# Optimization experiments

Measured on AMD Instinct MI355X. Metric: run time of the kernel, lower is better.

## Reference

```python
import jax, jax.numpy as jnp
import numpy as np

B, S, H, I, SI, E, TOPK = 2, 1024, 1024, 512, 2048, 8, 2


def setup_inputs() -> dict:
    key = jax.random.key(0)
    ks = jax.random.split(key, 8)
    w = 0.02
    return {
        "hidden_states": jax.random.normal(ks[0], (B, S, H), jnp.float32),
        "router_weight": jax.random.normal(ks[1], (E, H), jnp.float32) * w,
        "gate_up_proj": jax.random.normal(ks[2], (E, 2 * I, H), jnp.float32) * w,
        "down_proj": jax.random.normal(ks[3], (E, H, I), jnp.float32) * w,
        "shared_gate_w": jax.random.normal(ks[4], (SI, H), jnp.float32) * w,
        "shared_up_w": jax.random.normal(ks[5], (SI, H), jnp.float32) * w,
        "shared_down_w": jax.random.normal(ks[6], (H, SI), jnp.float32) * w,
        "shared_expert_gate_w": jax.random.normal(ks[7], (1, H), jnp.float32) * w,
    }


def reference(hidden_states, router_weight, gate_up_proj, down_proj,
              shared_gate_w, shared_up_w, shared_down_w, shared_expert_gate_w):
    b, s, h = hidden_states.shape
    x = hidden_states.reshape(-1, h)  # [T, H]

    # shared expert (SwiGLU)
    shared = (jax.nn.silu(x @ shared_gate_w.T) * (x @ shared_up_w.T)) @ shared_down_w.T  # [T, H]

    # top-k softmax router (softmax in fp32, renormalized top-k weights)
    logits = x @ router_weight.T  # [T, E]
    probs = jax.nn.softmax(logits.astype(jnp.float32), axis=-1)
    top_v, top_i = jax.lax.top_k(probs, TOPK)
    top_v = (top_v / jnp.sum(top_v, axis=-1, keepdims=True)).astype(logits.dtype)  # [T, K]

    # combine weights per (token, expert): sum over k of routing weight * one_hot
    cw = jnp.sum(jax.nn.one_hot(top_i, E, dtype=top_v.dtype) * top_v[..., None], axis=1)  # [T, E]

    # grouped-expert SwiGLU (dense compute, masked combine == gather/scatter math)
    gu = jnp.einsum('th,eih->eti', x, gate_up_proj)  # [E, T, 2I]
    gate, up = jnp.split(gu, 2, axis=-1)
    act = jax.nn.silu(gate) * up  # [E, T, I]
    per_expert = jnp.einsum('eti,ehi->eth', act, down_proj)  # [E, T, H]
    expert_out = jnp.einsum('eth,te->th', per_expert, cw)  # [T, H]

    out = expert_out + jax.nn.sigmoid(x @ shared_expert_gate_w.T) * shared
    return out.reshape(b, s, h)
```

## Files before the change

kernel.cpp:

```cpp
#include <hip/hip_runtime.h>

#define T_TOK 2048
#define H_DIM 1024
#define I_DIM 512
#define SI_DIM 2048
#define E_NUM 8
#define NSLOT 4096

typedef __attribute__((ext_vector_type(8))) short short8;
typedef __attribute__((ext_vector_type(4))) float floatx4;

__device__ inline unsigned short f2bf(float f) {
  unsigned u = __builtin_bit_cast(unsigned, f);
  u = (u + 0x7FFFu + ((u >> 16) & 1u)) >> 16;
  return (unsigned short)u;
}
__device__ inline float bf2f(unsigned short u) {
  return __builtin_bit_cast(float, (unsigned)u << 16);
}

__device__ inline void gl_lds16(const void* g, void* l) {
  __builtin_amdgcn_global_load_lds(
      (const __attribute__((address_space(1))) unsigned int*)g,
      (__attribute__((address_space(3))) unsigned int*)l, 16, 0, 0);
}

__global__ __launch_bounds__(256) void cast_router(
    const float* __restrict__ x, const float* __restrict__ rw,
    const float* __restrict__ segw,
    const float* __restrict__ s1, const float* __restrict__ s2,
    const float* __restrict__ s3, const float* __restrict__ s4,
    const float* __restrict__ s5,
    unsigned short* __restrict__ d0, unsigned short* __restrict__ d1,
    unsigned short* __restrict__ d2, unsigned short* __restrict__ d3,
    unsigned short* __restrict__ d4, unsigned short* __restrict__ d5,
    int* __restrict__ top2, float2* __restrict__ w01, float* __restrict__ sg) {
  const int bid = blockIdx.x;
  if (bid < 512) {
    int t = bid * 4 + (threadIdx.x >> 6);
    int lane = threadIdx.x & 63;
    const float* xt = x + (long)t * H_DIM;
    float xv[16];
#pragma unroll
    for (int j = 0; j < 16; ++j) xv[j] = xt[j * 64 + lane];
    float dots[9];
#pragma unroll
    for (int e = 0; e < 8; ++e) {
      const float* w = rw + e * H_DIM;
      float s = 0.f;
#pragma unroll
      for (int j = 0; j < 16; ++j) s += xv[j] * w[j * 64 + lane];
      dots[e] = s;
    }
    {
      float s = 0.f;
#pragma unroll
      for (int j = 0; j < 16; ++j) s += xv[j] * segw[j * 64 + lane];
      dots[8] = s;
    }
#pragma unroll
    for (int off = 32; off > 0; off >>= 1) {
#pragma unroll
      for (int e = 0; e < 9; ++e) dots[e] += __shfl_xor(dots[e], off, 64);
    }
    if (lane == 0) {
      int e0 = 0;
      for (int e = 1; e < 8; ++e)
        if (dots[e] > dots[e0]) e0 = e;
      int e1 = (e0 == 0) ? 1 : 0;
      for (int e = 0; e < 8; ++e)
        if (e != e0 && dots[e] > dots[e1]) e1 = e;
      float p1 = expf(dots[e1] - dots[e0]);
      top2[t] = e0 | (e1 << 8);
      w01[t] = make_float2(1.f / (1.f + p1), p1 / (1.f + p1));
      sg[t] = 1.f / (1.f + expf(-dots[8]));
    }
  } else {
    long g = (long)(bid - 512) * 256 + threadIdx.x;
    const float* s;
    unsigned short* d;
    long off;
    if (g < 524288L)       { s = x;  d = d0; off = g; }
    else if (g < 2621440L) { s = s1; d = d1; off = g - 524288L; }
    else if (g < 3670016L) { s = s2; d = d2; off = g - 2621440L; }
    else if (g < 4194304L) { s = s3; d = d3; off = g - 3670016L; }
    else if (g < 4718592L) { s = s4; d = d4; off = g - 4194304L; }
    else                   { s = s5; d = d5; off = g - 4718592L; }
    float4 v = ((const float4*)s)[off];
    ushort4 o;
    o.x = f2bf(v.x); o.y = f2bf(v.y); o.z = f2bf(v.z); o.w = f2bf(v.w);
    ((ushort4*)d)[off] = o;
  }
}

__global__ __launch_bounds__(256) void build_lists(
    const int* __restrict__ top2, int* __restrict__ cnt, int* __restrict__ ebase,
    int* __restrict__ slot_token, int* __restrict__ tok_slot) {
  const int e = blockIdx.x;
  const int tid = threadIdx.x;
  const int lane = tid & 63, wid = tid >> 6;
  __shared__ int wsum[4], wbelow[4];
  const int base_t = tid * 8;
  int mk[8], kk[8];
  int c = 0, below = 0;
#pragma unroll
  for (int j = 0; j < 8; ++j) {
    int p = top2[base_t + j];
    int e0 = p & 0xFF, e1 = (p >> 8) & 0xFF;
    below += (e0 < e) + (e1 < e);
    int m = 0, k = 0;
    if (e0 == e) { m = 1; k = 0; }
    else if (e1 == e) { m = 1; k = 1; }
    mk[j] = m; kk[j] = k;
    c += m;
  }
  int inc = c;
#pragma unroll
  for (int off = 1; off < 64; off <<= 1) {
    int n = __shfl_up(inc, off, 64);
    if (lane >= off) inc += n;
  }
  int bsum = below;
#pragma unroll
  for (int off = 32; off > 0; off >>= 1) bsum += __shfl_xor(bsum, off, 64);
  if (lane == 63) wsum[wid] = inc;
  if (lane == 0) wbelow[wid] = bsum;
  __syncthreads();
  int woff = 0;
#pragma unroll
  for (int i = 0; i < 4; ++i)
    if (i < wid) woff += wsum[i];
  int baseE = wbelow[0] + wbelow[1] + wbelow[2] + wbelow[3];
  int pos = baseE + woff + inc - c;
#pragma unroll
  for (int j = 0; j < 8; ++j) {
    if (mk[j]) {
      slot_token[pos] = base_t + j;
      tok_slot[2 * (base_t + j) + kk[j]] = pos;
      pos++;
    }
  }
  if (tid == 255) cnt[e] = woff + inc;
  if (tid == 0) ebase[e] = baseE;
}

template <bool GATHER, int BN>
__device__ __forceinline__ void swiglu_body(
    char* smem, int bx, int by, int e,
    const unsigned short* __restrict__ A, const unsigned short* __restrict__ Bg,
    const unsigned short* __restrict__ Bu, unsigned short* __restrict__ Out,
    const int* __restrict__ slot_token, const int* __restrict__ cnt,
    const int* __restrict__ ebase, int N, int K, long estrideB) {
  constexpr int BM = 128, BK = 32;
  constexpr int NT = BN / 32;
  constexpr int BCH = BN / 64;
  constexpr int ATILE = BM * BK;
  constexpr int BTILE = BN * BK;
  const int tid = threadIdx.x;
  const int lane = tid & 63;
  const int wid = tid >> 6;
  const int wm = wid & 1;
  const int wn = wid >> 1;
  const int m0 = by * BM;
  const int n0 = bx * BN;
  int Meff = 0, baseE = 0;
  if (GATHER) {
    Meff = cnt[e];
    if (m0 >= Meff) return;
    baseE = ebase[e];
  }
  const unsigned short* BgE = Bg + (long)e * estrideB;
  const unsigned short* BuE = Bu + (long)e * estrideB;

  unsigned short* As = (unsigned short*)smem;
  unsigned short* Bgs = As + 2 * ATILE;
  unsigned short* Bus = Bgs + 2 * BTILE;

  const int lrow = lane >> 2;
  const int lcol = (((lane & 3) ^ ((lrow >> 1) & 3)) << 4);

  const char* aP[2];
#pragma unroll
  for (int i = 0; i < 2; ++i) {
    int m = m0 + wid * 32 + i * 16 + lrow;
    long row;
    if (GATHER) {
      int mm = (m < Meff - 1) ? m : (Meff - 1);
      row = slot_token[baseE + mm];
    } else {
      row = m;
    }
    aP[i] = (const char*)A + row * (long)(K * 2) + lcol;
  }
  const char* bgP[BCH];
  const char* buP[BCH];
#pragma unroll
  for (int i = 0; i < BCH; ++i) {
    int n = n0 + wid * (16 * BCH) + i * 16 + lrow;
    bgP[i] = (const char*)BgE + (long)n * (K * 2) + lcol;
    buP[i] = (const char*)BuE + (long)n * (K * 2) + lcol;
  }

  floatx4 accG[4][NT], accU[4][NT];
  floatx4 zero = {0.f, 0.f, 0.f, 0.f};
#pragma unroll
  for (int i = 0; i < 4; ++i)
#pragma unroll
    for (int j = 0; j < NT; ++j) { accG[i][j] = zero; accU[i][j] = zero; }

  const int ar = lane & 15;
  const int aksw = (((lane >> 4) ^ ((ar >> 1) & 3)) << 3);

  auto stage = [&](int p, int k0) {
#pragma unroll
    for (int i = 0; i < 2; ++i)
      gl_lds16(aP[i] + (long)k0 * 2, &As[p * ATILE + (wid * 32 + i * 16) * BK]);
#pragma unroll
    for (int i = 0; i < BCH; ++i) {
      gl_lds16(bgP[i] + (long)k0 * 2,
               &Bgs[p * BTILE + (wid * 16 * BCH + i * 16) * BK]);
      gl_lds16(buP[i] + (long)k0 * 2,
               &Bus[p * BTILE + (wid * 16 * BCH + i * 16) * BK]);
    }
  };

  stage(0, 0);
  const int NI = K / BK;
  for (int i = 0; i < NI; ++i) {
    __syncthreads();
    if (i + 1 < NI) stage((i + 1) & 1, (i + 1) * BK);
    const unsigned short* Ab = &As[(i & 1) * ATILE];
    const unsigned short* Gb = &Bgs[(i & 1) * BTILE];
    const unsigned short* Ub = &Bus[(i & 1) * BTILE];
    short8 af[4], bgf[NT], buf2[NT];
#pragma unroll
    for (int tm = 0; tm < 4; ++tm)
      af[tm] = *(const short8*)&Ab[(wm * 64 + tm * 16 + ar) * BK + aksw];
#pragma unroll
    for (int tn = 0; tn < NT; ++tn) {
      bgf[tn] = *(const short8*)&Gb[(wn * (BN / 2) + tn * 16 + ar) * BK + aksw];
      buf2[tn] = *(const short8*)&Ub[(wn * (BN / 2) + tn * 16 + ar) * BK + aksw];
    }
#pragma unroll
    for (int tm = 0; tm < 4; ++tm)
#pragma unroll
      for (int tn = 0; tn < NT; ++tn) {
        accG[tm][tn] = __builtin_amdgcn_mfma_f32_16x16x32_bf16(af[tm], bgf[tn], accG[tm][tn], 0, 0, 0);
        accU[tm][tn] = __builtin_amdgcn_mfma_f32_16x16x32_bf16(af[tm], buf2[tn], accU[tm][tn], 0, 0, 0);
      }
  }

#pragma unroll
  for (int tm = 0; tm < 4; ++tm)
#pragma unroll
    for (int tn = 0; tn < NT; ++tn)
#pragma unroll
      for (int r = 0; r < 4; ++r) {
        int row = m0 + wm * 64 + tm * 16 + (lane >> 4) * 4 + r;
        int col = n0 + wn * (BN / 2) + tn * 16 + (lane & 15);
        if (!GATHER || row < Meff) {
          float g = accG[tm][tn][r];
          float u = accU[tm][tn][r];
          float act = g / (1.f + expf(-g)) * u;
          Out[(long)(baseE + row) * N + col] = f2bf(act);
        }
      }
}

__global__ __launch_bounds__(256, 2) void swiglu_fused(
    const unsigned short* __restrict__ xb, const unsigned short* __restrict__ sgate,
    const unsigned short* __restrict__ sup, unsigned short* __restrict__ act_s,
    const unsigned short* __restrict__ gup, unsigned short* __restrict__ act_e,
    const int* __restrict__ slot_token, const int* __restrict__ cnt,
    const int* __restrict__ ebase) {
  __shared__ __align__(16) char smem[49152];
  int bid = blockIdx.x;
  if (bid < 256) {
    swiglu_body<false, 128>(smem, bid & 15, bid >> 4, 0, xb, sgate, sup, act_s,
                            nullptr, nullptr, nullptr, SI_DIM, H_DIM, 0);
  } else {
    int b2 = bid - 256;
    int e = b2 >> 7;
    int rem = b2 & 127;
    swiglu_body<true, 64>(smem, rem & 7, rem >> 3, e, xb, gup,
                          gup + (long)I_DIM * H_DIM, act_e, slot_token, cnt,
                          ebase, I_DIM, H_DIM, (long)2 * I_DIM * H_DIM);
  }
}

template <int MODE>
__device__ __forceinline__ void down_body(
    char* smem, int bx, int by, int e,
    const unsigned short* __restrict__ A, const unsigned short* __restrict__ B,
    float* __restrict__ OutF, unsigned short* __restrict__ OutB,
    const int* __restrict__ ebase, const int* __restrict__ cnt,
    int N, int Kstride, int kbeg, int kcnt, long estrideB) {
  constexpr int BM = 128, BN = 128, BK = 32;
  constexpr int ATILE = BM * BK;
  constexpr int BTILE = BN * BK;
  const int tid = threadIdx.x;
  const int lane = tid & 63;
  const int wid = tid >> 6;
  const int wm = wid & 1;
  const int wn = wid >> 1;
  const int m0 = by * BM;
  const int n0 = bx * BN;
  int Meff = 0, baseE = 0;
  if (MODE == 1) {
    Meff = cnt[e];
    if (m0 >= Meff) return;
    baseE = ebase[e];
  }
  const unsigned short* BE = B + (long)e * estrideB;

  unsigned short* As = (unsigned short*)smem;
  unsigned short* Bs = As + 2 * ATILE;

  const int lrow = lane >> 2;
  const int lcol = (((lane & 3) ^ ((lrow >> 1) & 3)) << 4);

  const char* aP[2];
  const char* bP[2];
#pragma unroll
  for (int i = 0; i < 2; ++i) {
    int m = m0 + wid * 32 + i * 16 + lrow;
    long arow;
    if (MODE == 1) {
      int mm = (m < Meff - 1) ? m : (Meff - 1);
      arow = baseE + mm;
    } else {
      arow = m;
    }
    aP[i] = (const char*)A + arow * (long)(Kstride * 2) + (long)kbeg * 2 + lcol;
    int n = n0 + wid * 32 + i * 16 + lrow;
    bP[i] = (const char*)BE + (long)n * (Kstride * 2) + (long)kbeg * 2 + lcol;
  }

  floatx4 acc[4][4];
  floatx4 zero = {0.f, 0.f, 0.f, 0.f};
#pragma unroll
  for (int i = 0; i < 4; ++i)
#pragma unroll
    for (int j = 0; j < 4; ++j) acc[i][j] = zero;

  const int ar = lane & 15;
  const int aksw = (((lane >> 4) ^ ((ar >> 1) & 3)) << 3);

  auto stage = [&](int p, int k0) {
#pragma unroll
    for (int i = 0; i < 2; ++i) {
      gl_lds16(aP[i] + (long)k0 * 2, &As[p * ATILE + (wid * 32 + i * 16) * BK]);
      gl_lds16(bP[i] + (long)k0 * 2, &Bs[p * BTILE + (wid * 32 + i * 16) * BK]);
    }
  };

  stage(0, 0);
  const int NI = kcnt / BK;
  for (int i = 0; i < NI; ++i) {
    __syncthreads();
    if (i + 1 < NI) stage((i + 1) & 1, (i + 1) * BK);
    const unsigned short* Ab = &As[(i & 1) * ATILE];
    const unsigned short* Bb = &Bs[(i & 1) * BTILE];
    short8 af[4], bf[4];
#pragma unroll
    for (int tm = 0; tm < 4; ++tm)
      af[tm] = *(const short8*)&Ab[(wm * 64 + tm * 16 + ar) * BK + aksw];
#pragma unroll
    for (int tn = 0; tn < 4; ++tn)
      bf[tn] = *(const short8*)&Bb[(wn * 64 + tn * 16 + ar) * BK + aksw];
#pragma unroll
    for (int tm = 0; tm < 4; ++tm)
#pragma unroll
      for (int tn = 0; tn < 4; ++tn)
        acc[tm][tn] = __builtin_amdgcn_mfma_f32_16x16x32_bf16(af[tm], bf[tn], acc[tm][tn], 0, 0, 0);
  }

#pragma unroll
  for (int tm = 0; tm < 4; ++tm)
#pragma unroll
    for (int r = 0; r < 4; ++r) {
      int row = m0 + wm * 64 + tm * 16 + (lane >> 4) * 4 + r;
#pragma unroll
      for (int tn = 0; tn < 4; ++tn) {
        int col = n0 + wn * 64 + tn * 16 + (lane & 15);
        float v = acc[tm][tn][r];
        if (MODE == 0) {
          OutF[(long)row * N + col] = v;
        } else if (MODE == 2) {
          OutB[(long)row * N + col] = f2bf(v);
        } else if (row < Meff) {
          OutB[(long)(baseE + row) * N + col] = f2bf(v);
        }
      }
    }
}

__global__ __launch_bounds__(256, 2) void down_fused(
    const unsigned short* __restrict__ act_s, const unsigned short* __restrict__ sdown,
    float* __restrict__ out, unsigned short* __restrict__ spart,
    const unsigned short* __restrict__ act_e, const unsigned short* __restrict__ downw,
    unsigned short* __restrict__ eout, const int* __restrict__ ebase,
    const int* __restrict__ cnt) {
  __shared__ __align__(16) char smem[32768];
  int bid = blockIdx.x;
  if (bid < 256) {
    int ks = bid >> 7;
    int rem = bid & 127;
    if (ks == 0)
      down_body<0>(smem, rem & 7, rem >> 3, 0, act_s, sdown, out, nullptr,
                   nullptr, nullptr, H_DIM, SI_DIM, 0, 1024, 0);
    else
      down_body<2>(smem, rem & 7, rem >> 3, 0, act_s, sdown, nullptr, spart,
                   nullptr, nullptr, H_DIM, SI_DIM, 1024, 1024, 0);
  } else {
    int b2 = bid - 256;
    int e = b2 >> 7;
    int rem = b2 & 127;
    down_body<1>(smem, rem & 7, rem >> 3, e, act_e, downw, nullptr, eout,
                 ebase, cnt, H_DIM, I_DIM, 0, I_DIM, (long)H_DIM * I_DIM);
  }
}

__global__ __launch_bounds__(256) void combine_kernel(
    float* __restrict__ out, const unsigned short* __restrict__ spart,
    const unsigned short* __restrict__ eout, const float* __restrict__ sg,
    const float2* __restrict__ w01, const int* __restrict__ tok_slot) {
  int t = blockIdx.x;
  int c = threadIdx.x;
  float sgr = sg[t];
  float2 wr = w01[t];
  int s0 = tok_slot[2 * t];
  int s1 = tok_slot[2 * t + 1];
  ushort4 p1 = ((const ushort4*)(spart + (long)t * H_DIM))[c];
  ushort4 e0 = ((const ushort4*)(eout + (long)s0 * H_DIM))[c];
  ushort4 e1 = ((const ushort4*)(eout + (long)s1 * H_DIM))[c];
  float4* op = &((float4*)(out + (long)t * H_DIM))[c];
  float4 o = *op;
  o.x = sgr * (o.x + bf2f(p1.x)) + wr.x * bf2f(e0.x) + wr.y * bf2f(e1.x);
  o.y = sgr * (o.y + bf2f(p1.y)) + wr.x * bf2f(e0.y) + wr.y * bf2f(e1.y);
  o.z = sgr * (o.z + bf2f(p1.z)) + wr.x * bf2f(e0.z) + wr.y * bf2f(e1.z);
  o.w = sgr * (o.w + bf2f(p1.w)) + wr.x * bf2f(e0.w) + wr.y * bf2f(e1.w);
  *op = o;
}

extern "C" void kernel_launch(void* const* d_in, const int* in_sizes, int n_in,
                              void* d_out, int out_size, void* d_ws, size_t ws_size,
                              hipStream_t stream) {
  const float* x = (const float*)d_in[0];
  const float* rw = (const float*)d_in[1];
  const float* gup = (const float*)d_in[2];
  const float* dwn = (const float*)d_in[3];
  const float* sgw = (const float*)d_in[4];
  const float* suw = (const float*)d_in[5];
  const float* sdw = (const float*)d_in[6];
  const float* segw = (const float*)d_in[7];
  float* out = (float*)d_out;

  char* w = (char*)d_ws;
  unsigned short* xb = (unsigned short*)(w + 0);
  unsigned short* gup_b = (unsigned short*)(w + 4194304L);
  unsigned short* down_b = (unsigned short*)(w + 20971520L);
  unsigned short* sgate_b = (unsigned short*)(w + 29360128L);
  unsigned short* sup_b = (unsigned short*)(w + 33554432L);
  unsigned short* sdown_b = (unsigned short*)(w + 37748736L);
  unsigned short* act_s = (unsigned short*)(w + 41943040L);
  unsigned short* act_e = (unsigned short*)(w + 50331648L);
  unsigned short* eout = (unsigned short*)(w + 54525952L);
  float* sg = (float*)(w + 62914560L);
  int* top2 = (int*)(w + 62922752L);
  float2* w01 = (float2*)(w + 62930944L);
  int* cnt = (int*)(w + 62947328L);
  int* ebase = (int*)(w + 62947584L);
  int* slot_token = (int*)(w + 62947840L);
  int* tok_slot = (int*)(w + 62964224L);
  unsigned short* spart = xb;

  cast_router<<<20992, 256, 0, stream>>>(x, rw, segw, gup, dwn, sgw, suw, sdw,
                                         xb, gup_b, down_b, sgate_b, sup_b,
                                         sdown_b, top2, w01, sg);
  build_lists<<<E_NUM, 256, 0, stream>>>(top2, cnt, ebase, slot_token, tok_slot);
  swiglu_fused<<<1280, 256, 0, stream>>>(xb, sgate_b, sup_b, act_s, gup_b,
                                         act_e, slot_token, cnt, ebase);
  down_fused<<<1280, 256, 0, stream>>>(act_s, sdown_b, out, spart, act_e,
                                       down_b, eout, ebase, cnt);
  combine_kernel<<<T_TOK, 256, 0, stream>>>(out, spart, eout, sg, w01, tok_slot);
}
```

Baseline: 209.3 us.

## Overlap down-proj weight casts with SwiGLU GEMM and widen expert tiles

Moves the fp32-to-bf16 cast of the expert down_proj and shared down weights out of the initial cast kernel and into extra blocks of the SwiGLU kernel, so that memory-bound conversion can run alongside the MFMA GEMM blocks instead of serializing before them. The expert SwiGLU path also moves from BN=64 to BN=128 tiles, which halves the number of expert blocks and increases reuse of the gathered A tile. The trade-off is that the larger tiles hold more accumulator registers per wave, and the cast blocks compete with the GEMM blocks for CU slots and memory bandwidth.

Result: no change. 206.3 us (-1.5%).

```diff
diff --git a/kernel.cpp b/kernel.cpp
--- a/kernel.cpp
+++ b/kernel.cpp
@@ -28,12 +28,11 @@
 __global__ __launch_bounds__(256) void cast_router(
     const float* __restrict__ x, const float* __restrict__ rw,
     const float* __restrict__ segw,
-    const float* __restrict__ s1, const float* __restrict__ s2,
-    const float* __restrict__ s3, const float* __restrict__ s4,
-    const float* __restrict__ s5,
+    const float* __restrict__ s1,
+    const float* __restrict__ s3,
+    const float* __restrict__ s4,
     unsigned short* __restrict__ d0, unsigned short* __restrict__ d1,
-    unsigned short* __restrict__ d2, unsigned short* __restrict__ d3,
-    unsigned short* __restrict__ d4, unsigned short* __restrict__ d5,
+    unsigned short* __restrict__ d3, unsigned short* __restrict__ d4,
     int* __restrict__ top2, float2* __restrict__ w01, float* __restrict__ sg) {
   const int bid = blockIdx.x;
   if (bid < 512) {
@@ -82,10 +81,8 @@
     long off;
     if (g < 524288L)       { s = x;  d = d0; off = g; }
     else if (g < 2621440L) { s = s1; d = d1; off = g - 524288L; }
-    else if (g < 3670016L) { s = s2; d = d2; off = g - 2621440L; }
-    else if (g < 4194304L) { s = s3; d = d3; off = g - 3670016L; }
-    else if (g < 4718592L) { s = s4; d = d4; off = g - 4194304L; }
-    else                   { s = s5; d = d5; off = g - 4718592L; }
+    else if (g < 3145728L) { s = s3; d = d3; off = g - 2621440L; }
+    else                   { s = s4; d = d4; off = g - 3145728L; }
     float4 v = ((const float4*)s)[off];
     ushort4 o;
     o.x = f2bf(v.x); o.y = f2bf(v.y); o.z = f2bf(v.z); o.w = f2bf(v.w);
@@ -144,16 +141,14 @@
   if (tid == 0) ebase[e] = baseE;
 }
 
-template <bool GATHER, int BN>
+template <bool GATHER>
 __device__ __forceinline__ void swiglu_body(
     char* smem, int bx, int by, int e,
     const unsigned short* __restrict__ A, const unsigned short* __restrict__ Bg,
     const unsigned short* __restrict__ Bu, unsigned short* __restrict__ Out,
     const int* __restrict__ slot_token, const int* __restrict__ cnt,
     const int* __restrict__ ebase, int N, int K, long estrideB) {
-  constexpr int BM = 128, BK = 32;
-  constexpr int NT = BN / 32;
-  constexpr int BCH = BN / 64;
+  constexpr int BM = 128, BN = 128, BK = 32;
   constexpr int ATILE = BM * BK;
   constexpr int BTILE = BN * BK;
   const int tid = threadIdx.x;
@@ -180,6 +175,8 @@
   const int lcol = (((lane & 3) ^ ((lrow >> 1) & 3)) << 4);
 
   const char* aP[2];
+  const char* bgP[2];
+  const char* buP[2];
 #pragma unroll
   for (int i = 0; i < 2; ++i) {
     int m = m0 + wid * 32 + i * 16 + lrow;
@@ -191,36 +188,27 @@
       row = m;
     }
     aP[i] = (const char*)A + row * (long)(K * 2) + lcol;
-  }
-  const char* bgP[BCH];
-  const char* buP[BCH];
-#pragma unroll
-  for (int i = 0; i < BCH; ++i) {
-    int n = n0 + wid * (16 * BCH) + i * 16 + lrow;
+    int n = n0 + wid * 32 + i * 16 + lrow;
     bgP[i] = (const char*)BgE + (long)n * (K * 2) + lcol;
     buP[i] = (const char*)BuE + (long)n * (K * 2) + lcol;
   }
 
-  floatx4 accG[4][NT], accU[4][NT];
+  floatx4 accG[4][4], accU[4][4];
   floatx4 zero = {0.f, 0.f, 0.f, 0.f};
 #pragma unroll
   for (int i = 0; i < 4; ++i)
 #pragma unroll
-    for (int j = 0; j < NT; ++j) { accG[i][j] = zero; accU[i][j] = zero; }
+    for (int j = 0; j < 4; ++j) { accG[i][j] = zero; accU[i][j] = zero; }
 
   const int ar = lane & 15;
   const int aksw = (((lane >> 4) ^ ((ar >> 1) & 3)) << 3);
 
   auto stage = [&](int p, int k0) {
 #pragma unroll
-    for (int i = 0; i < 2; ++i)
+    for (int i = 0; i < 2; ++i) {
       gl_lds16(aP[i] + (long)k0 * 2, &As[p * ATILE + (wid * 32 + i * 16) * BK]);
-#pragma unroll
-    for (int i = 0; i < BCH; ++i) {
-      gl_lds16(bgP[i] + (long)k0 * 2,
-               &Bgs[p * BTILE + (wid * 16 * BCH + i * 16) * BK]);
-      gl_lds16(buP[i] + (long)k0 * 2,
-               &Bus[p * BTILE + (wid * 16 * BCH + i * 16) * BK]);
+      gl_lds16(bgP[i] + (long)k0 * 2, &Bgs[p * BTILE + (wid * 32 + i * 16) * BK]);
+      gl_lds16(buP[i] + (long)k0 * 2, &Bus[p * BTILE + (wid * 32 + i * 16) * BK]);
     }
   };
 
@@ -232,19 +220,19 @@
     const unsigned short* Ab = &As[(i & 1) * ATILE];
     const unsigned short* Gb = &Bgs[(i & 1) * BTILE];
     const unsigned short* Ub = &Bus[(i & 1) * BTILE];
-    short8 af[4], bgf[NT], buf2[NT];
+    short8 af[4], bgf[4], buf2[4];
 #pragma unroll
     for (int tm = 0; tm < 4; ++tm)
       af[tm] = *(const short8*)&Ab[(wm * 64 + tm * 16 + ar) * BK + aksw];
 #pragma unroll
-    for (int tn = 0; tn < NT; ++tn) {
-      bgf[tn] = *(const short8*)&Gb[(wn * (BN / 2) + tn * 16 + ar) * BK + aksw];
-      buf2[tn] = *(const short8*)&Ub[(wn * (BN / 2) + tn * 16 + ar) * BK + aksw];
+    for (int tn = 0; tn < 4; ++tn) {
+      bgf[tn] = *(const short8*)&Gb[(wn * 64 + tn * 16 + ar) * BK + aksw];
+      buf2[tn] = *(const short8*)&Ub[(wn * 64 + tn * 16 + ar) * BK + aksw];
     }
 #pragma unroll
     for (int tm = 0; tm < 4; ++tm)
 #pragma unroll
-      for (int tn = 0; tn < NT; ++tn) {
+      for (int tn = 0; tn < 4; ++tn) {
         accG[tm][tn] = __builtin_amdgcn_mfma_f32_16x16x32_bf16(af[tm], bgf[tn], accG[tm][tn], 0, 0, 0);
         accU[tm][tn] = __builtin_amdgcn_mfma_f32_16x16x32_bf16(af[tm], buf2[tn], accU[tm][tn], 0, 0, 0);
       }
@@ -253,11 +241,11 @@
 #pragma unroll
   for (int tm = 0; tm < 4; ++tm)
 #pragma unroll
-    for (int tn = 0; tn < NT; ++tn)
+    for (int tn = 0; tn < 4; ++tn)
 #pragma unroll
       for (int r = 0; r < 4; ++r) {
         int row = m0 + wm * 64 + tm * 16 + (lane >> 4) * 4 + r;
-        int col = n0 + wn * (BN / 2) + tn * 16 + (lane & 15);
+        int col = n0 + wn * 64 + tn * 16 + (lane & 15);
         if (!GATHER || row < Meff) {
           float g = accG[tm][tn][r];
           float u = accU[tm][tn][r];
@@ -272,19 +260,32 @@
     const unsigned short* __restrict__ sup, unsigned short* __restrict__ act_s,
     const unsigned short* __restrict__ gup, unsigned short* __restrict__ act_e,
     const int* __restrict__ slot_token, const int* __restrict__ cnt,
-    const int* __restrict__ ebase) {
+    const int* __restrict__ ebase,
+    const float* __restrict__ dwn_f, const float* __restrict__ sdw_f,
+    unsigned short* __restrict__ down_b, unsigned short* __restrict__ sdown_b) {
   __shared__ __align__(16) char smem[49152];
   int bid = blockIdx.x;
   if (bid < 256) {
-    swiglu_body<false, 128>(smem, bid & 15, bid >> 4, 0, xb, sgate, sup, act_s,
-                            nullptr, nullptr, nullptr, SI_DIM, H_DIM, 0);
+    swiglu_body<false>(smem, bid & 15, bid >> 4, 0, xb, sgate, sup, act_s,
+                       nullptr, nullptr, nullptr, SI_DIM, H_DIM, 0);
+  } else if (bid < 768) {
+    int b2 = bid - 256;
+    int e = b2 >> 6;
+    int rem = b2 & 63;
+    swiglu_body<true>(smem, rem & 3, rem >> 2, e, xb, gup,
+                      gup + (long)I_DIM * H_DIM, act_e, slot_token, cnt,
+                      ebase, I_DIM, H_DIM, (long)2 * I_DIM * H_DIM);
   } else {
-    int b2 = bid - 256;
-    int e = b2 >> 7;
-    int rem = b2 & 127;
-    swiglu_body<true, 64>(smem, rem & 7, rem >> 3, e, xb, gup,
-                          gup + (long)I_DIM * H_DIM, act_e, slot_token, cnt,
-                          ebase, I_DIM, H_DIM, (long)2 * I_DIM * H_DIM);
+    long g = (long)(bid - 768) * 256 + threadIdx.x;
+    const float* s;
+    unsigned short* d;
+    long off;
+    if (g < 1048576L) { s = dwn_f; d = down_b; off = g; }
+    else              { s = sdw_f; d = sdown_b; off = g - 1048576L; }
+    float4 v = ((const float4*)s)[off];
+    ushort4 o;
+    o.x = f2bf(v.x); o.y = f2bf(v.y); o.z = f2bf(v.z); o.w = f2bf(v.w);
+    ((ushort4*)d)[off] = o;
   }
 }
 
@@ -475,12 +476,13 @@
   int* tok_slot = (int*)(w + 62964224L);
   unsigned short* spart = xb;
 
-  cast_router<<<20992, 256, 0, stream>>>(x, rw, segw, gup, dwn, sgw, suw, sdw,
-                                         xb, gup_b, down_b, sgate_b, sup_b,
-                                         sdown_b, top2, w01, sg);
+  cast_router<<<14848, 256, 0, stream>>>(x, rw, segw, gup, sgw, suw,
+                                         xb, gup_b, sgate_b, sup_b,
+                                         top2, w01, sg);
   build_lists<<<E_NUM, 256, 0, stream>>>(top2, cnt, ebase, slot_token, tok_slot);
-  swiglu_fused<<<1280, 256, 0, stream>>>(xb, sgate_b, sup_b, act_s, gup_b,
-                                         act_e, slot_token, cnt, ebase);
+  swiglu_fused<<<6912, 256, 0, stream>>>(xb, sgate_b, sup_b, act_s, gup_b,
+                                         act_e, slot_token, cnt, ebase,
+                                         dwn, sdw, down_b, sdown_b);
   down_fused<<<1280, 256, 0, stream>>>(act_s, sdown_b, out, spart, act_e,
                                        down_b, eout, ebase, cnt);
   combine_kernel<<<T_TOK, 256, 0, stream>>>(out, spart, eout, sg, w01, tok_slot);
```
